# Kernel tuning notes

Measured on AMD Instinct MI355X. Metric: run time of the kernel, lower is better.

Reference implementation:

```python
import jax, jax.numpy as jnp
import numpy as np

VOCAB = 65
N_EMBD = 32
HEAD = 16
BLOCK = 8
B = 65536


def setup_inputs() -> dict:
    key = jax.random.key(0)
    ks = jax.random.split(key, 12)
    idx = jax.random.randint(ks[0], (B, BLOCK), 0, VOCAB)
    targets = jax.random.randint(ks[1], (B, BLOCK), 0, VOCAB)
    s = 0.02
    tok_emb = jax.random.normal(ks[2], (VOCAB, N_EMBD), jnp.float32) * s
    pos_emb = jax.random.normal(ks[3], (BLOCK, N_EMBD), jnp.float32) * s
    Wk = jax.random.normal(ks[4], (N_EMBD, HEAD), jnp.float32) * s
    bk = jnp.zeros((HEAD,), jnp.float32)
    Wq = jax.random.normal(ks[5], (N_EMBD, HEAD), jnp.float32) * s
    bq = jnp.zeros((HEAD,), jnp.float32)
    Wv = jax.random.normal(ks[6], (N_EMBD, HEAD), jnp.float32) * s
    bv = jnp.zeros((HEAD,), jnp.float32)
    Wlm = jax.random.normal(ks[7], (HEAD, VOCAB), jnp.float32) * s
    blm = jnp.zeros((VOCAB,), jnp.float32)
    return {"idx": idx, "targets": targets, "tok_emb": tok_emb, "pos_emb": pos_emb,
            "Wk": Wk, "bk": bk, "Wq": Wq, "bq": bq, "Wv": Wv, "bv": bv,
            "Wlm": Wlm, "blm": blm}


def reference(idx, targets, tok_emb, pos_emb, Wk, bk, Wq, bq, Wv, bv, Wlm, blm):
    Bsz, T = idx.shape
    x = tok_emb[idx] + pos_emb[None, :T, :]                  # (B,T,C)
    k = x @ Wk + bk                                          # (B,T,H)
    q = x @ Wq + bq
    wei = jnp.einsum('bth,bsh->bts', q, k) * (HEAD ** -0.5)  # (B,T,T)
    tril = jnp.tril(jnp.ones((T, T), bool))
    wei = jnp.where(tril[None], wei, -jnp.inf)
    # NOTE: original torch code uses F.softmax(wei, dim=1) — over the QUERY axis.
    wei = jax.nn.softmax(wei, axis=1)
    v = x @ Wv + bv
    attn = jnp.einsum('bts,bsh->bth', wei, v)                # (B,T,H)
    logits = attn @ Wlm + blm                                # (B,T,V)
    logits_flat = logits.reshape(Bsz * T, VOCAB)
    tgt_flat = targets.reshape(Bsz * T)
    logp = jax.nn.log_softmax(logits_flat, axis=-1)
    loss = -jnp.mean(jnp.take_along_axis(logp, tgt_flat[:, None], axis=-1))
    return logits_flat, loss
```

## Files before the change

### kernel.cpp

```cpp
#include <hip/hip_runtime.h>
#include <hip/hip_bf16.h>

#define NVOC 65
#define NE   32
#define HD   16
#define NB   65536
#define NROWS (NB * 8)
#define NLOG  (NROWS * NVOC)


static __device__ __forceinline__ float readlane_f(float v, int l) {
  return __uint_as_float(__builtin_amdgcn_readlane(__float_as_uint(v), l));
}

__global__ __launch_bounds__(1024) void bigram_tables(
    const float* __restrict__ tok, const float* __restrict__ pos,
    const float* __restrict__ Wk, const float* __restrict__ bk,
    const float* __restrict__ Wq, const float* __restrict__ bq,
    const float* __restrict__ Wv, const float* __restrict__ bv,
    const float* __restrict__ Wlm, float* __restrict__ ws)
{
  __shared__ float S[8416];
  const int tid = threadIdx.x;
  if (tid == 0) ws[0] = 0.f;
  for (int o = tid; o < 2080; o += 1024) S[o] = tok[o];
  for (int o = tid; o < 256;  o += 1024) S[2080 + o] = pos[o];
  for (int o = tid; o < 512;  o += 1024) {
    S[2336 + o] = Wq[o]; S[2848 + o] = Wk[o]; S[3360 + o] = Wv[o];
  }
  for (int o = tid; o < 1040; o += 1024) S[3872 + o] = Wlm[o];
  __syncthreads();

  for (int o = tid; o < 1168; o += 1024) {
    if (o < 1040) {
      const int a = o >> 4, h = o & 15;
      float sq = 0.f, sk = 0.f, sv = 0.f;
      #pragma unroll
      for (int c = 0; c < NE; ++c) {
        const float e = S[a*32 + c];
        sq = fmaf(e, S[2336 + c*16 + h], sq);
        sk = fmaf(e, S[2848 + c*16 + h], sk);
        sv = fmaf(e, S[3360 + c*16 + h], sv);
      }
      S[4912 + o] = sq; S[5952 + o] = sk; S[6992 + o] = sv;
    } else {
      const int o2 = o - 1040, t = o2 >> 4, h = o2 & 15;
      float sq = bq[h], sk = bk[h], sv = bv[h];
      #pragma unroll
      for (int c = 0; c < NE; ++c) {
        const float e = S[2080 + t*32 + c];
        sq = fmaf(e, S[2336 + c*16 + h], sq);
        sk = fmaf(e, S[2848 + c*16 + h], sk);
        sv = fmaf(e, S[3360 + c*16 + h], sv);
      }
      S[8032 + o2] = sq; S[8160 + o2] = sk; S[8288 + o2] = sv;
    }
  }
  __syncthreads();

  float* wsTab = ws + 16;
  for (int o = tid; o < 10074; o += 1024) {
    float r = 0.f; int dst;
    if (o < 4225) {
      const int a = o / 65, b = o % 65;
      #pragma unroll
      for (int h = 0; h < HD; ++h) r = fmaf(S[4912 + a*16 + h], S[5952 + b*16 + h], r);
      r *= 0.25f; dst = o;
    } else if (o < 4745) {
      const int o2 = o - 4225, a = o2 >> 3, s2 = o2 & 7;
      #pragma unroll
      for (int h = 0; h < HD; ++h) r = fmaf(S[4912 + a*16 + h], S[8160 + s2*16 + h], r);
      r *= 0.25f; dst = 8450 + o2;
    } else if (o < 5265) {
      const int o2 = o - 4745, t2 = o2 / 65, b = o2 % 65;
      #pragma unroll
      for (int h = 0; h < HD; ++h) r = fmaf(S[8032 + t2*16 + h], S[5952 + b*16 + h], r);
      r *= 0.25f; dst = 8970 + o2;
    } else if (o < 5329) {
      const int o2 = o - 5265, t2 = o2 >> 3, s2 = o2 & 7;
      #pragma unroll
      for (int h = 0; h < HD; ++h) r = fmaf(S[8032 + t2*16 + h], S[8160 + s2*16 + h], r);
      r *= 0.25f; dst = 9490 + o2;
    } else if (o < 9554) {
      const int o2 = o - 5329, a = o2 / 65, j = o2 % 65;
      #pragma unroll
      for (int h = 0; h < HD; ++h) r = fmaf(S[6992 + a*16 + h], S[3872 + h*65 + j], r);
      dst = 4225 + o2;
    } else {
      const int o2 = o - 9554, s2 = o2 / 65, j = o2 % 65;
      #pragma unroll
      for (int h = 0; h < HD; ++h) r = fmaf(S[8288 + s2*16 + h], S[3872 + h*65 + j], r);
      dst = o;
    }
    wsTab[dst] = r;
  }
}

__global__ __launch_bounds__(512, 6) void bigram_main(
    const int* __restrict__ idx, const int* __restrict__ tgt,
    const float* __restrict__ blm, const float* __restrict__ ws,
    float* __restrict__ wsacc, float* __restrict__ out)
{
  __shared__ __align__(16) float S[10074];
  __shared__ float red[8];
  const int tid = threadIdx.x;
  const float* wsTab = ws + 16;
  {
    const float4* t4 = (const float4*)wsTab;
    float4* s4 = (float4*)S;
    for (int o = tid; o < 2518; o += 512) s4[o] = t4[o];
    if (tid < 2) S[10072 + tid] = wsTab[10072 + tid];
  }
  const int lane = tid & 63;
  const int w    = tid >> 6;
  const int t    = lane >> 3;
  const int s    = lane & 7;
  const float blmj  = blm[lane];
  const float blm64 = blm[64];
  const int gw = blockIdx.x * 8 + w;
  const int iv = idx[gw*64 + lane];
  const int tv = tgt[gw*64 + lane];
  __syncthreads();

  const float g4 = S[9490 + lane];
  float pvl[8], pvl64[8];
  #pragma unroll
  for (int k = 0; k < 8; ++k) {
    pvl[k]   = S[9554 + k*65 + lane];
    pvl64[k] = S[9554 + k*65 + 64];
  }

  float acc_lsm = 0.f, acc_tl = 0.f;
  for (int itb = 0; itb < 8; ++itb) {
    const int base = itb * 8;
    const int av  = __shfl(iv, base + s);
    const int a_t = __shfl(iv, base + t);
    float wr = S[a_t*65 + av] + S[8450 + a_t*8 + s] + S[8970 + t*65 + av] + g4;
    float e = (t >= s) ? __expf(wr) : 0.f;
    float sm = e;
    sm += __shfl_xor(sm, 8); sm += __shfl_xor(sm, 16); sm += __shfl_xor(sm, 32);
    const float wsm = __fdividef(e, sm);
    float Ms[8], Ms64[8];
    #pragma unroll
    for (int k = 0; k < 8; ++k) {
      const int ak = __builtin_amdgcn_readlane(iv, base + k);
      Ms[k]   = S[4225 + ak*65 + lane] + pvl[k];
      Ms64[k] = S[4225 + ak*65 + 64]  + pvl64[k];
    }
    const int rowbase = (gw*8 + itb) * 520;
    float ee[8];
    #pragma unroll
    for (int tt = 0; tt < 8; ++tt) {
      float lg = blmj, lg64 = blm64;
      #pragma unroll
      for (int k = 0; k < 8; ++k) {
        const float wk = readlane_f(wsm, tt*8 + k);
        lg   = fmaf(wk, Ms[k],   lg);
        lg64 = fmaf(wk, Ms64[k], lg64);
      }
      out[rowbase + tt*65 + lane] = lg;
      if (lane == 63) out[rowbase + tt*65 + 64] = lg64;
      float x = __expf(lg);
      if (lane == 63) x += __expf(lg64);
      ee[tt] = x;
      const int tg  = __builtin_amdgcn_readlane(tv, base + tt);
      const int tgc = tg < 64 ? tg : 0;
      const float l_at_tg = readlane_f(lg, tgc);
      acc_tl += (tg < 64) ? l_at_tg : lg64;
    }
    #pragma unroll
    for (int tt = 0; tt < 8; ++tt) {
      ee[tt] += __shfl_xor(ee[tt], 1);
      ee[tt] += __shfl_xor(ee[tt], 2);
      ee[tt] += __shfl_xor(ee[tt], 4);
    }
    const int u = lane & 7;
    float r01 = (u & 1) ? ee[1] : ee[0];
    float r23 = (u & 1) ? ee[3] : ee[2];
    float r45 = (u & 1) ? ee[5] : ee[4];
    float r67 = (u & 1) ? ee[7] : ee[6];
    float r03 = (u & 2) ? r23 : r01;
    float r47 = (u & 2) ? r67 : r45;
    float r   = (u & 4) ? r47 : r03;
    r += __shfl_xor(r, 8); r += __shfl_xor(r, 16); r += __shfl_xor(r, 32);
    acc_lsm += __logf(r);
  }
  float v = acc_lsm * 0.125f - acc_tl * 0.015625f;
  v += __shfl_xor(v, 1); v += __shfl_xor(v, 2);  v += __shfl_xor(v, 4);
  v += __shfl_xor(v, 8); v += __shfl_xor(v, 16); v += __shfl_xor(v, 32);
  if (lane == 0) red[w] = v;
  __syncthreads();
  if (tid == 0) {
    float acc = red[0] + red[1] + red[2] + red[3] + red[4] + red[5] + red[6] + red[7];
    atomicAdd(wsacc, acc);
  }
}

__global__ void bigram_fin(const float* __restrict__ ws, float* __restrict__ out) {
  if (threadIdx.x == 0) out[NLOG] = ws[0] * (1.0f / (float)NROWS);
}

extern "C" void kernel_launch(void* const* d_in, const int* in_sizes, int n_in,
                              void* d_out, int out_size, void* d_ws, size_t ws_size,
                              hipStream_t stream) {
  const int* idx = (const int*)d_in[0];
  const int* tgt = (const int*)d_in[1];
  float* ws = (float*)d_ws;
  float* out = (float*)d_out;

  bigram_tables<<<1, 1024, 0, stream>>>((const float*)d_in[2], (const float*)d_in[3],
                                        (const float*)d_in[4], (const float*)d_in[5],
                                        (const float*)d_in[6], (const float*)d_in[7],
                                        (const float*)d_in[8], (const float*)d_in[9],
                                        (const float*)d_in[10], ws);
  bigram_main<<<1024, 512, 0, stream>>>(idx, tgt, (const float*)d_in[11], ws, ws, out);
  bigram_fin<<<1, 1, 0, stream>>>(ws, out);
}
```

Before: 208.5 us.

## Fuse table precompute into main kernel and replace atomic loss with two-stage reduction

Each block now recomputes the projected token/position tables and pairwise score and output tables in its own shared memory, so the single-block table-building kernel and its serial dependency go away. The atomicAdd into a zeroed workspace slot is replaced by per-block partial sums written to the workspace and summed by a final 1024-thread kernel. The cost is that all 1024 blocks redo about 10k short dot products plus the projections, and shared memory grows to about 58KB per block with launch bounds lowered to 4 blocks per SM.

```diff
diff --git a/kernel.cpp b/kernel.cpp
--- a/kernel.cpp
+++ b/kernel.cpp
@@ -1,5 +1,4 @@
 #include <hip/hip_runtime.h>
-#include <hip/hip_bf16.h>
 
 #define NVOC 65
 #define NE   32
@@ -8,30 +7,54 @@
 #define NROWS (NB * 8)
 #define NLOG  (NROWS * NVOC)
 
+#define TQ_  10076
+#define TK_  11116
+#define TV_  12156
+#define WLM_ 13196
+#define PQ_  14236
+#define PK_  14364
+#define PV_  14492
+#define SEND 14620
 
 static __device__ __forceinline__ float readlane_f(float v, int l) {
   return __uint_as_float(__builtin_amdgcn_readlane(__float_as_uint(v), l));
 }
 
-__global__ __launch_bounds__(1024) void bigram_tables(
+__global__ __launch_bounds__(512, 4) void bigram_all(
+    const int* __restrict__ idx, const int* __restrict__ tgt,
     const float* __restrict__ tok, const float* __restrict__ pos,
     const float* __restrict__ Wk, const float* __restrict__ bk,
     const float* __restrict__ Wq, const float* __restrict__ bq,
     const float* __restrict__ Wv, const float* __restrict__ bv,
-    const float* __restrict__ Wlm, float* __restrict__ ws)
+    const float* __restrict__ Wlm, const float* __restrict__ blm,
+    float* __restrict__ ws, float* __restrict__ out)
 {
-  __shared__ float S[8416];
-  const int tid = threadIdx.x;
-  if (tid == 0) ws[0] = 0.f;
-  for (int o = tid; o < 2080; o += 1024) S[o] = tok[o];
-  for (int o = tid; o < 256;  o += 1024) S[2080 + o] = pos[o];
-  for (int o = tid; o < 512;  o += 1024) {
-    S[2336 + o] = Wq[o]; S[2848 + o] = Wk[o]; S[3360 + o] = Wv[o];
-  }
-  for (int o = tid; o < 1040; o += 1024) S[3872 + o] = Wlm[o];
-  __syncthreads();
-
-  for (int o = tid; o < 1168; o += 1024) {
+  __shared__ __align__(16) float S[SEND];
+  __shared__ float red[8];
+  const int tid  = threadIdx.x;
+  const int lane = tid & 63;
+  const int w    = tid >> 6;
+  const int t    = lane >> 3;
+  const int s    = lane & 7;
+  const int gw   = blockIdx.x * 8 + w;
+  const int iv = idx[gw*64 + lane];
+  const int tv = tgt[gw*64 + lane];
+  const float blmj  = blm[lane];
+  const float blm64 = blm[64];
+
+  {
+    float4* s4 = (float4*)S;
+    const float4* t4;
+    t4 = (const float4*)tok; for (int o = tid; o < 520; o += 512) s4[o] = t4[o];
+    t4 = (const float4*)pos; if (tid < 64)  s4[520 + tid] = t4[tid];
+    t4 = (const float4*)Wq;  if (tid < 128) s4[584 + tid] = t4[tid];
+    t4 = (const float4*)Wk;  if (tid < 128) s4[712 + tid] = t4[tid];
+    t4 = (const float4*)Wv;  if (tid < 128) s4[840 + tid] = t4[tid];
+    t4 = (const float4*)Wlm; for (int o = tid; o < 260; o += 512) s4[3299 + o] = t4[o];
+  }
+  __syncthreads();
+
+  for (int o = tid; o < 1168; o += 512) {
     if (o < 1040) {
       const int a = o >> 4, h = o & 15;
       float sq = 0.f, sk = 0.f, sv = 0.f;
@@ -42,84 +65,55 @@
         sk = fmaf(e, S[2848 + c*16 + h], sk);
         sv = fmaf(e, S[3360 + c*16 + h], sv);
       }
-      S[4912 + o] = sq; S[5952 + o] = sk; S[6992 + o] = sv;
+      S[TQ_ + o] = sq; S[TK_ + o] = sk; S[TV_ + o] = sv;
     } else {
-      const int o2 = o - 1040, t = o2 >> 4, h = o2 & 15;
+      const int o2 = o - 1040, tp = o2 >> 4, h = o2 & 15;
       float sq = bq[h], sk = bk[h], sv = bv[h];
       #pragma unroll
       for (int c = 0; c < NE; ++c) {
-        const float e = S[2080 + t*32 + c];
+        const float e = S[2080 + tp*32 + c];
         sq = fmaf(e, S[2336 + c*16 + h], sq);
         sk = fmaf(e, S[2848 + c*16 + h], sk);
         sv = fmaf(e, S[3360 + c*16 + h], sv);
       }
-      S[8032 + o2] = sq; S[8160 + o2] = sk; S[8288 + o2] = sv;
-    }
-  }
-  __syncthreads();
-
-  float* wsTab = ws + 16;
-  for (int o = tid; o < 10074; o += 1024) {
-    float r = 0.f; int dst;
+      S[PQ_ + o2] = sq; S[PK_ + o2] = sk; S[PV_ + o2] = sv;
+    }
+  }
+  __syncthreads();
+
+  for (int o = tid; o < 10074; o += 512) {
+    float r = 0.f;
     if (o < 4225) {
       const int a = o / 65, b = o % 65;
       #pragma unroll
-      for (int h = 0; h < HD; ++h) r = fmaf(S[4912 + a*16 + h], S[5952 + b*16 + h], r);
-      r *= 0.25f; dst = o;
-    } else if (o < 4745) {
-      const int o2 = o - 4225, a = o2 >> 3, s2 = o2 & 7;
-      #pragma unroll
-      for (int h = 0; h < HD; ++h) r = fmaf(S[4912 + a*16 + h], S[8160 + s2*16 + h], r);
-      r *= 0.25f; dst = 8450 + o2;
-    } else if (o < 5265) {
-      const int o2 = o - 4745, t2 = o2 / 65, b = o2 % 65;
-      #pragma unroll
-      for (int h = 0; h < HD; ++h) r = fmaf(S[8032 + t2*16 + h], S[5952 + b*16 + h], r);
-      r *= 0.25f; dst = 8970 + o2;
-    } else if (o < 5329) {
-      const int o2 = o - 5265, t2 = o2 >> 3, s2 = o2 & 7;
-      #pragma unroll
-      for (int h = 0; h < HD; ++h) r = fmaf(S[8032 + t2*16 + h], S[8160 + s2*16 + h], r);
-      r *= 0.25f; dst = 9490 + o2;
+      for (int h = 0; h < HD; ++h) r = fmaf(S[TQ_ + a*16 + h], S[TK_ + b*16 + h], r);
+      r *= 0.25f;
+    } else if (o < 8450) {
+      const int o2 = o - 4225, a = o2 / 65, j = o2 % 65;
+      #pragma unroll
+      for (int h = 0; h < HD; ++h) r = fmaf(S[TV_ + a*16 + h], S[WLM_ + h*65 + j], r);
+    } else if (o < 8970) {
+      const int o2 = o - 8450, a = o2 >> 3, s2 = o2 & 7;
+      #pragma unroll
+      for (int h = 0; h < HD; ++h) r = fmaf(S[TQ_ + a*16 + h], S[PK_ + s2*16 + h], r);
+      r *= 0.25f;
+    } else if (o < 9490) {
+      const int o2 = o - 8970, t2 = o2 / 65, b = o2 % 65;
+      #pragma unroll
+      for (int h = 0; h < HD; ++h) r = fmaf(S[PQ_ + t2*16 + h], S[TK_ + b*16 + h], r);
+      r *= 0.25f;
     } else if (o < 9554) {
-      const int o2 = o - 5329, a = o2 / 65, j = o2 % 65;
-      #pragma unroll
-      for (int h = 0; h < HD; ++h) r = fmaf(S[6992 + a*16 + h], S[3872 + h*65 + j], r);
-      dst = 4225 + o2;
+      const int o2 = o - 9490, t2 = o2 >> 3, s2 = o2 & 7;
+      #pragma unroll
+      for (int h = 0; h < HD; ++h) r = fmaf(S[PQ_ + t2*16 + h], S[PK_ + s2*16 + h], r);
+      r *= 0.25f;
     } else {
       const int o2 = o - 9554, s2 = o2 / 65, j = o2 % 65;
       #pragma unroll
-      for (int h = 0; h < HD; ++h) r = fmaf(S[8288 + s2*16 + h], S[3872 + h*65 + j], r);
-      dst = o;
-    }
-    wsTab[dst] = r;
-  }
-}
-
-__global__ __launch_bounds__(512, 6) void bigram_main(
-    const int* __restrict__ idx, const int* __restrict__ tgt,
-    const float* __restrict__ blm, const float* __restrict__ ws,
-    float* __restrict__ wsacc, float* __restrict__ out)
-{
-  __shared__ __align__(16) float S[10074];
-  __shared__ float red[8];
-  const int tid = threadIdx.x;
-  const float* wsTab = ws + 16;
-  {
-    const float4* t4 = (const float4*)wsTab;
-    float4* s4 = (float4*)S;
-    for (int o = tid; o < 2518; o += 512) s4[o] = t4[o];
-    if (tid < 2) S[10072 + tid] = wsTab[10072 + tid];
-  }
-  const int lane = tid & 63;
-  const int w    = tid >> 6;
-  const int t    = lane >> 3;
-  const int s    = lane & 7;
-  const float blmj  = blm[lane];
-  const float blm64 = blm[64];
-  const int gw = blockIdx.x * 8 + w;
-  const int iv = idx[gw*64 + lane];
-  const int tv = tgt[gw*64 + lane];
+      for (int h = 0; h < HD; ++h) r = fmaf(S[PV_ + s2*16 + h], S[WLM_ + h*65 + j], r);
+    }
+    S[o] = r;
+  }
   __syncthreads();
 
   const float g4 = S[9490 + lane];
@@ -191,28 +185,39 @@
   if (lane == 0) red[w] = v;
   __syncthreads();
   if (tid == 0) {
-    float acc = red[0] + red[1] + red[2] + red[3] + red[4] + red[5] + red[6] + red[7];
-    atomicAdd(wsacc, acc);
-  }
-}
-
-__global__ void bigram_fin(const float* __restrict__ ws, float* __restrict__ out) {
-  if (threadIdx.x == 0) out[NLOG] = ws[0] * (1.0f / (float)NROWS);
+    ws[blockIdx.x] = red[0] + red[1] + red[2] + red[3]
+                   + red[4] + red[5] + red[6] + red[7];
+  }
+}
+
+__global__ __launch_bounds__(1024) void bigram_fin2(
+    const float* __restrict__ ws, float* __restrict__ out)
+{
+  __shared__ float r[16];
+  const int tid = threadIdx.x;
+  float v = ws[tid];
+  v += __shfl_xor(v, 1); v += __shfl_xor(v, 2);  v += __shfl_xor(v, 4);
+  v += __shfl_xor(v, 8); v += __shfl_xor(v, 16); v += __shfl_xor(v, 32);
+  if ((tid & 63) == 0) r[tid >> 6] = v;
+  __syncthreads();
+  if (tid == 0) {
+    float a = 0.f;
+    #pragma unroll
+    for (int i = 0; i < 16; ++i) a += r[i];
+    out[NLOG] = a * (1.0f / (float)NROWS);
+  }
 }
 
 extern "C" void kernel_launch(void* const* d_in, const int* in_sizes, int n_in,
                               void* d_out, int out_size, void* d_ws, size_t ws_size,
                               hipStream_t stream) {
-  const int* idx = (const int*)d_in[0];
-  const int* tgt = (const int*)d_in[1];
-  float* ws = (float*)d_ws;
-  float* out = (float*)d_out;
-
-  bigram_tables<<<1, 1024, 0, stream>>>((const float*)d_in[2], (const float*)d_in[3],
-                                        (const float*)d_in[4], (const float*)d_in[5],
-                                        (const float*)d_in[6], (const float*)d_in[7],
-                                        (const float*)d_in[8], (const float*)d_in[9],
-                                        (const float*)d_in[10], ws);
-  bigram_main<<<1024, 512, 0, stream>>>(idx, tgt, (const float*)d_in[11], ws, ws, out);
-  bigram_fin<<<1, 1, 0, stream>>>(ws, out);
-}
+  bigram_all<<<1024, 512, 0, stream>>>(
+      (const int*)d_in[0], (const int*)d_in[1],
+      (const float*)d_in[2], (const float*)d_in[3],
+      (const float*)d_in[4], (const float*)d_in[5],
+      (const float*)d_in[6], (const float*)d_in[7],
+      (const float*)d_in[8], (const float*)d_in[9],
+      (const float*)d_in[10], (const float*)d_in[11],
+      (float*)d_ws, (float*)d_out);
+  bigram_fin2<<<1, 1024, 0, stream>>>((const float*)d_ws, (float*)d_out);
+}
```

After: 222.3 us. +6.6%, slower.
